# Kernel optimization log

Measured on AMD Instinct MI355X. Metric: run time of the kernel, lower is better.

The kernel has to match this reference:

```python
import jax, jax.numpy as jnp
import numpy as np

TAU = 0.5  # init tau
EPS = 1e-8  # F.cosine_similarity eps


def setup_inputs() -> dict:
    key = jax.random.key(0)
    k1, k2 = jax.random.split(key)
    N, D, NUM_CLASSES = 4096, 1024, 128
    layer_embeds = jax.random.normal(k1, (N, D), dtype=jnp.float32)
    y_true = jax.random.randint(k2, (N,), 0, NUM_CLASSES, dtype=jnp.int64)
    return {"layer_embeds": layer_embeds, "y_true": y_true}


def reference(layer_embeds, y_true):
    N = layer_embeds.shape[0]
    # batched cosine similarity, scaled like the original: (cos + 1) * 0.5 * tau
    norms = jnp.maximum(jnp.linalg.norm(layer_embeds, axis=1), EPS)  # [N]
    cos = (layer_embeds @ layer_embeds.T) / (norms[:, None] * norms[None, :])  # [N, N]
    S = (cos + 1.0) * 0.5 * TAU

    same = y_true[:, None] == y_true[None, :]  # [N, N]
    eye = jnp.eye(N, dtype=bool)
    pos_mask = same & ~eye            # same-label pairs, j != i
    neg_mask = ~same                  # different-label pairs (diag excluded since same there)

    # column 0: first positive (in j order), else stays 0
    has_pos = pos_mask.any(axis=1)
    first_pos = jnp.argmax(pos_mask, axis=1)
    pos_val = jnp.where(has_pos, S[jnp.arange(N), first_pos], 0.0)  # [N]

    # negatives fill columns 1.. in j order: col = 1 + (#negatives with j' < j)
    negi = neg_mask.astype(jnp.int32)
    col = 1 + jnp.cumsum(negi, axis=1) - negi  # [N, N]
    W = 2 * N  # pad one dummy column for non-negative entries
    cols = jnp.where(neg_mask, col, W - 1)
    rows = jnp.broadcast_to(jnp.arange(N)[:, None], (N, N))
    loss_temp = jnp.zeros((N, W), dtype=jnp.float32)
    loss_temp = loss_temp.at[rows, cols].set(jnp.where(neg_mask, S, 0.0))
    loss_temp = loss_temp.at[:, 0].set(pos_val)
    loss_temp = loss_temp[:, : 2 * N - 1]  # [N, 2N-1], matches torch buffer

    # -log_softmax, take column 0, sum over rows, divide by N
    lse = jax.nn.logsumexp(loss_temp, axis=1)  # [N]
    loss = jnp.sum(lse - loss_temp[:, 0]) / N
    return loss
```

## Files before the change

kernel.cpp:

```cpp
#include <hip/hip_runtime.h>
#include <hip/hip_bf16.h>
#include <math.h>

#define NN 4096
#define DD 1024
#define NCLS 128
#define TAU 0.5f
#define EPSV 1e-8f
#define NB_GEMM 528

typedef __bf16 bf16;
typedef __bf16 bf16x8 __attribute__((ext_vector_type(8)));
typedef __bf16 bf16x4 __attribute__((ext_vector_type(4)));
typedef float f32x4 __attribute__((ext_vector_type(4)));

__device__ __forceinline__ void gl2lds16(const void* g, void* l) {
    __builtin_amdgcn_global_load_lds(
        (const __attribute__((address_space(1))) void*)g,
        (__attribute__((address_space(3))) void*)l,
        16, 0, 0);
}

__global__ __launch_bounds__(256) void k_prep(const float* __restrict__ X,
                                              const int* __restrict__ y,
                                              bf16* __restrict__ Xn,
                                              float* __restrict__ rsum,
                                              float* __restrict__ posv,
                                              int* __restrict__ cnt,
                                              int* __restrict__ fpos) {
    const int t = threadIdx.x;
    if (blockIdx.x == 0) {
        __shared__ int sc[NCLS], s1[NCLS], s2[NCLS];
        if (t < NCLS) { sc[t] = 0; s1[t] = 0x7fffffff; s2[t] = 0x7fffffff; }
        __syncthreads();
        int yv[16];
#pragma unroll
        for (int k = 0; k < 16; ++k) {
            int i = t + k * 256;
            yv[k] = y[i];
            atomicAdd(&sc[yv[k]], 1);
            atomicMin(&s1[yv[k]], i);
        }
        __syncthreads();
#pragma unroll
        for (int k = 0; k < 16; ++k) {
            int i = t + k * 256;
            if (s1[yv[k]] != i) atomicMin(&s2[yv[k]], i);
        }
        __syncthreads();
#pragma unroll
        for (int k = 0; k < 16; ++k) {
            int i = t + k * 256;
            int c = yv[k];
            fpos[i] = (sc[c] >= 2) ? (s1[c] == i ? s2[c] : s1[c]) : -1;
        }
        if (t < NCLS) cnt[t] = sc[t];
        return;
    }
    const int w = t >> 6, lane = t & 63;
    const int row = (blockIdx.x - 1) * 4 + w;
    const float* xr = X + (size_t)row * DD;
    float4 v[4];
    float ss = 0.f;
#pragma unroll
    for (int c = 0; c < 4; ++c) {
        v[c] = *(const float4*)(xr + c * 256 + lane * 4);
        ss += v[c].x * v[c].x + v[c].y * v[c].y + v[c].z * v[c].z + v[c].w * v[c].w;
    }
#pragma unroll
    for (int m = 1; m < 64; m <<= 1) ss += __shfl_xor(ss, m, 64);
    float rn = 1.f / fmaxf(sqrtf(ss), EPSV);
    if (lane == 0) { rsum[row] = 0.f; posv[row] = 0.f; }
#pragma unroll
    for (int c = 0; c < 4; ++c) {
        bf16x4 o;
        o.x = (bf16)(v[c].x * rn);
        o.y = (bf16)(v[c].y * rn);
        o.z = (bf16)(v[c].z * rn);
        o.w = (bf16)(v[c].w * rn);
        *(bf16x4*)(Xn + (size_t)row * DD + c * 256 + lane * 4) = o;
    }
}

__global__ __launch_bounds__(256) void k_gemm(const bf16* __restrict__ Xn,
                                              const int* __restrict__ y,
                                              const int* __restrict__ fpos,
                                              float* __restrict__ rowsum,
                                              float* __restrict__ posv) {
    __shared__ __align__(16) bf16 As[128 * 32];
    __shared__ __align__(16) bf16 Bs[128 * 32];
    __shared__ int yA[128], yB[128], fA[128], fB[128];

    int id = (blockIdx.x & 7) * 66 + (blockIdx.x >> 3);
    float ff = sqrtf((float)(8 * id + 1));
    int bj = (int)((ff - 1.f) * 0.5f);
    if (bj * (bj + 1) / 2 > id) bj--;
    if ((bj + 1) * (bj + 2) / 2 <= id) bj++;
    int bi = id - bj * (bj + 1) / 2;
    const int rowA0 = bi * 128;
    const int rowB0 = bj * 128;
    const bool diag = (bi == bj);

    const int tid = threadIdx.x;
    if (tid < 128) { yA[tid] = y[rowA0 + tid]; fA[tid] = fpos[rowA0 + tid]; }
    else { yB[tid - 128] = y[rowB0 + tid - 128]; fB[tid - 128] = fpos[rowB0 + tid - 128]; }

    const int lane = tid & 63;
    const int w = tid >> 6;
    const int wm = w & 1, wn = w >> 1;
    const int lr = lane >> 4, lc = lane & 15;

    f32x4 acc[4][4];
#pragma unroll
    for (int i = 0; i < 4; ++i)
#pragma unroll
        for (int j = 0; j < 4; ++j) acc[i][j] = (f32x4){0.f, 0.f, 0.f, 0.f};

    const int r = tid >> 2;
    const int g = tid & 3;
    const int kg = g ^ ((r >> 1) & 3);
    const bf16* gA0 = Xn + (size_t)(rowA0 + r) * DD + kg * 8;
    const bf16* gA1 = gA0 + (size_t)64 * DD;
    const bf16* gB0 = Xn + (size_t)(rowB0 + r) * DD + kg * 8;
    const bf16* gB1 = gB0 + (size_t)64 * DD;
    bf16* lA0 = As + tid * 8;
    bf16* lA1 = As + 64 * 32 + tid * 8;
    bf16* lB0 = Bs + tid * 8;
    bf16* lB1 = Bs + 64 * 32 + tid * 8;

    const int sw = (lc >> 1) & 3;

    for (int k0 = 0; k0 < DD; k0 += 32) {
        __syncthreads();
        gl2lds16(gA0 + k0, lA0);
        gl2lds16(gA1 + k0, lA1);
        gl2lds16(gB0 + k0, lB0);
        gl2lds16(gB1 + k0, lB1);
        __syncthreads();

        bf16x8 af[4], bfr[4];
#pragma unroll
        for (int mt = 0; mt < 4; ++mt)
            af[mt] = *(const bf16x8*)(As + (wm * 64 + mt * 16 + lc) * 32 + ((lr ^ sw) * 8));
#pragma unroll
        for (int nt = 0; nt < 4; ++nt)
            bfr[nt] = *(const bf16x8*)(Bs + (wn * 64 + nt * 16 + lc) * 32 + ((lr ^ sw) * 8));
#pragma unroll
        for (int mt = 0; mt < 4; ++mt)
#pragma unroll
            for (int nt = 0; nt < 4; ++nt)
                acc[mt][nt] = __builtin_amdgcn_mfma_f32_16x16x32_bf16(
                    af[mt], bfr[nt], acc[mt][nt], 0, 0, 0);
    }

    int cloc[4], ycol[4], fcol[4];
    bool pcol[4];
#pragma unroll
    for (int nt = 0; nt < 4; ++nt) {
        cloc[nt] = wn * 64 + nt * 16 + lc;
        ycol[nt] = yB[cloc[nt]];
        fcol[nt] = fB[cloc[nt]];
        pcol[nt] = ((unsigned)(fcol[nt] - rowA0) < 128u);
    }
    float colacc[4] = {0.f, 0.f, 0.f, 0.f};
#pragma unroll
    for (int mt = 0; mt < 4; ++mt) {
#pragma unroll
        for (int rr = 0; rr < 4; ++rr) {
            int rloc = wm * 64 + mt * 16 + lr * 4 + rr;
            int rglob = rowA0 + rloc;
            int yrow = yA[rloc];
            int fprow = fA[rloc];
            bool prow = ((unsigned)(fprow - rowB0) < 128u);
            float s = 0.f;
#pragma unroll
            for (int nt = 0; nt < 4; ++nt) {
                float Sv = (acc[mt][nt][rr] + 1.f) * (0.5f * TAU);
                int cg = rowB0 + cloc[nt];
                if (prow && cg == fprow) posv[rglob] = Sv;
                if (pcol[nt] && fcol[nt] == rglob) posv[cg] = Sv;
                float e = (ycol[nt] != yrow) ? __expf(Sv) : 0.f;
                s += e;
                colacc[nt] += e;
            }
            s += __shfl_xor(s, 1, 16);
            s += __shfl_xor(s, 2, 16);
            s += __shfl_xor(s, 4, 16);
            s += __shfl_xor(s, 8, 16);
            if (lc == 0) atomicAdd(&rowsum[rglob], s);
        }
    }
    if (!diag) {
#pragma unroll
        for (int nt = 0; nt < 4; ++nt) {
            float cs = colacc[nt];
            cs += __shfl_xor(cs, 16, 64);
            cs += __shfl_xor(cs, 32, 64);
            if (lane < 16) atomicAdd(&rowsum[rowB0 + wn * 64 + nt * 16 + lane], cs);
        }
    }
}

__global__ __launch_bounds__(1024) void k_finalize(const float* __restrict__ rowsum,
                                                   const float* __restrict__ posv,
                                                   const int* __restrict__ y,
                                                   const int* __restrict__ cnt,
                                                   float* __restrict__ out) {
    int t = threadIdx.x;
    float acc = 0.f;
#pragma unroll
    for (int k = 0; k < 4; ++k) {
        int i = t + k * 1024;
        float pv = posv[i];
        float tot = rowsum[i] + __expf(pv) + (float)(NN - 2 + cnt[y[i]]);
        acc += logf(tot) - pv;
    }
#pragma unroll
    for (int m = 1; m < 64; m <<= 1) acc += __shfl_xor(acc, m, 64);
    __shared__ float wsum[16];
    int w = t >> 6, lane = t & 63;
    if (lane == 0) wsum[w] = acc;
    __syncthreads();
    if (t == 0) {
        float s = 0.f;
#pragma unroll
        for (int q = 0; q < 16; ++q) s += wsum[q];
        *out = s / (float)NN;
    }
}

extern "C" void kernel_launch(void* const* d_in, const int* in_sizes, int n_in,
                              void* d_out, int out_size, void* d_ws, size_t ws_size,
                              hipStream_t stream) {
    const float* X = (const float*)d_in[0];
    const int* y = (const int*)d_in[1];
    float* out = (float*)d_out;

    char* ws = (char*)d_ws;
    bf16* Xn    = (bf16*)ws;
    float* rsum = (float*)(ws + 8 * 1024 * 1024);
    float* posv = (float*)(ws + 8 * 1024 * 1024 + 16 * 1024);
    int* cnt    = (int*)(ws + 8 * 1024 * 1024 + 32 * 1024);
    int* fpos   = (int*)(ws + 8 * 1024 * 1024 + 36 * 1024);

    k_prep<<<dim3(NN / 4 + 1), 256, 0, stream>>>(X, y, Xn, rsum, posv, cnt, fpos);
    k_gemm<<<dim3(NB_GEMM), 256, 0, stream>>>(Xn, y, fpos, rsum, posv);
    k_finalize<<<dim3(1), 1024, 0, stream>>>(rsum, posv, y, cnt, out);
}
```

Baseline: 104.0 us.

## Double-buffer LDS tiles and split GEMM block across eight waves

The GEMM kernel now uses 512 threads (8 waves) per 128x128 tile. Each wave computes a 64x32 sub-tile instead of 64x64, which halves the accumulator registers per thread. The LDS tiles are double-buffered so the next K-slice is prefetched with global_load_lds while MFMAs run on the current one, leaving one barrier per iteration instead of two. This aims to hide global-load latency and raise occupancy, at the cost of twice the LDS use and more LDS fragment reads per MFMA.

```diff
diff --git a/kernel.cpp b/kernel.cpp
--- a/kernel.cpp
+++ b/kernel.cpp
@@ -82,13 +82,13 @@
     }
 }
 
-__global__ __launch_bounds__(256) void k_gemm(const bf16* __restrict__ Xn,
-                                              const int* __restrict__ y,
-                                              const int* __restrict__ fpos,
-                                              float* __restrict__ rowsum,
-                                              float* __restrict__ posv) {
-    __shared__ __align__(16) bf16 As[128 * 32];
-    __shared__ __align__(16) bf16 Bs[128 * 32];
+__global__ __launch_bounds__(512, 4) void k_gemm(const bf16* __restrict__ Xn,
+                                                 const int* __restrict__ y,
+                                                 const int* __restrict__ fpos,
+                                                 float* __restrict__ rowsum,
+                                                 float* __restrict__ posv) {
+    __shared__ __align__(16) bf16 As[2][128 * 32];
+    __shared__ __align__(16) bf16 Bs[2][128 * 32];
     __shared__ int yA[128], yB[128], fA[128], fB[128];
 
     int id = (blockIdx.x & 7) * 66 + (blockIdx.x >> 3);
@@ -103,66 +103,65 @@
 
     const int tid = threadIdx.x;
     if (tid < 128) { yA[tid] = y[rowA0 + tid]; fA[tid] = fpos[rowA0 + tid]; }
-    else { yB[tid - 128] = y[rowB0 + tid - 128]; fB[tid - 128] = fpos[rowB0 + tid - 128]; }
+    else if (tid < 256) { yB[tid - 128] = y[rowB0 + tid - 128]; fB[tid - 128] = fpos[rowB0 + tid - 128]; }
 
     const int lane = tid & 63;
     const int w = tid >> 6;
     const int wm = w & 1, wn = w >> 1;
     const int lr = lane >> 4, lc = lane & 15;
 
-    f32x4 acc[4][4];
+    f32x4 acc[4][2];
 #pragma unroll
     for (int i = 0; i < 4; ++i)
 #pragma unroll
-        for (int j = 0; j < 4; ++j) acc[i][j] = (f32x4){0.f, 0.f, 0.f, 0.f};
+        for (int j = 0; j < 2; ++j) acc[i][j] = (f32x4){0.f, 0.f, 0.f, 0.f};
 
     const int r = tid >> 2;
     const int g = tid & 3;
     const int kg = g ^ ((r >> 1) & 3);
-    const bf16* gA0 = Xn + (size_t)(rowA0 + r) * DD + kg * 8;
-    const bf16* gA1 = gA0 + (size_t)64 * DD;
-    const bf16* gB0 = Xn + (size_t)(rowB0 + r) * DD + kg * 8;
-    const bf16* gB1 = gB0 + (size_t)64 * DD;
-    bf16* lA0 = As + tid * 8;
-    bf16* lA1 = As + 64 * 32 + tid * 8;
-    bf16* lB0 = Bs + tid * 8;
-    bf16* lB1 = Bs + 64 * 32 + tid * 8;
+    const bf16* gA = Xn + (size_t)(rowA0 + r) * DD + kg * 8;
+    const bf16* gB = Xn + (size_t)(rowB0 + r) * DD + kg * 8;
+    const int loff = tid * 8;
 
     const int sw = (lc >> 1) & 3;
 
+    gl2lds16(gA, &As[0][loff]);
+    gl2lds16(gB, &Bs[0][loff]);
+    __syncthreads();
+
+    int cur = 0;
     for (int k0 = 0; k0 < DD; k0 += 32) {
-        __syncthreads();
-        gl2lds16(gA0 + k0, lA0);
-        gl2lds16(gA1 + k0, lA1);
-        gl2lds16(gB0 + k0, lB0);
-        gl2lds16(gB1 + k0, lB1);
-        __syncthreads();
-
-        bf16x8 af[4], bfr[4];
+        if (k0 + 32 < DD) {
+            gl2lds16(gA + k0 + 32, &As[cur ^ 1][loff]);
+            gl2lds16(gB + k0 + 32, &Bs[cur ^ 1][loff]);
+        }
+        bf16x8 af[4], bfr[2];
 #pragma unroll
         for (int mt = 0; mt < 4; ++mt)
-            af[mt] = *(const bf16x8*)(As + (wm * 64 + mt * 16 + lc) * 32 + ((lr ^ sw) * 8));
-#pragma unroll
-        for (int nt = 0; nt < 4; ++nt)
-            bfr[nt] = *(const bf16x8*)(Bs + (wn * 64 + nt * 16 + lc) * 32 + ((lr ^ sw) * 8));
+            af[mt] = *(const bf16x8*)(&As[cur][(wm * 64 + mt * 16 + lc) * 32 + ((lr ^ sw) * 8)]);
+#pragma unroll
+        for (int nt = 0; nt < 2; ++nt)
+            bfr[nt] = *(const bf16x8*)(&Bs[cur][(wn * 32 + nt * 16 + lc) * 32 + ((lr ^ sw) * 8)]);
 #pragma unroll
         for (int mt = 0; mt < 4; ++mt)
 #pragma unroll
-            for (int nt = 0; nt < 4; ++nt)
+            for (int nt = 0; nt < 2; ++nt)
                 acc[mt][nt] = __builtin_amdgcn_mfma_f32_16x16x32_bf16(
                     af[mt], bfr[nt], acc[mt][nt], 0, 0, 0);
-    }
-
-    int cloc[4], ycol[4], fcol[4];
-    bool pcol[4];
-#pragma unroll
-    for (int nt = 0; nt < 4; ++nt) {
-        cloc[nt] = wn * 64 + nt * 16 + lc;
+        __syncthreads();
+        cur ^= 1;
+    }
+
+    int cloc[2], ycol[2], fcol[2];
+    bool pcol[2];
+#pragma unroll
+    for (int nt = 0; nt < 2; ++nt) {
+        cloc[nt] = wn * 32 + nt * 16 + lc;
         ycol[nt] = yB[cloc[nt]];
         fcol[nt] = fB[cloc[nt]];
         pcol[nt] = ((unsigned)(fcol[nt] - rowA0) < 128u);
     }
-    float colacc[4] = {0.f, 0.f, 0.f, 0.f};
+    float colacc[2] = {0.f, 0.f};
 #pragma unroll
     for (int mt = 0; mt < 4; ++mt) {
 #pragma unroll
@@ -174,7 +173,7 @@
             bool prow = ((unsigned)(fprow - rowB0) < 128u);
             float s = 0.f;
 #pragma unroll
-            for (int nt = 0; nt < 4; ++nt) {
+            for (int nt = 0; nt < 2; ++nt) {
                 float Sv = (acc[mt][nt][rr] + 1.f) * (0.5f * TAU);
                 int cg = rowB0 + cloc[nt];
                 if (prow && cg == fprow) posv[rglob] = Sv;
@@ -192,11 +191,11 @@
     }
     if (!diag) {
 #pragma unroll
-        for (int nt = 0; nt < 4; ++nt) {
+        for (int nt = 0; nt < 2; ++nt) {
             float cs = colacc[nt];
             cs += __shfl_xor(cs, 16, 64);
             cs += __shfl_xor(cs, 32, 64);
-            if (lane < 16) atomicAdd(&rowsum[rowB0 + wn * 64 + nt * 16 + lane], cs);
+            if (lane < 16) atomicAdd(&rowsum[rowB0 + wn * 32 + nt * 16 + lane], cs);
         }
     }
 }
@@ -244,6 +243,6 @@
     int* fpos   = (int*)(ws + 8 * 1024 * 1024 + 36 * 1024);
 
     k_prep<<<dim3(NN / 4 + 1), 256, 0, stream>>>(X, y, Xn, rsum, posv, cnt, fpos);
-    k_gemm<<<dim3(NB_GEMM), 256, 0, stream>>>(Xn, y, fpos, rsum, posv);
+    k_gemm<<<dim3(NB_GEMM), 512, 0, stream>>>(Xn, y, fpos, rsum, posv);
     k_finalize<<<dim3(1), 1024, 0, stream>>>(rsum, posv, y, cnt, out);
 }
```

Result: slower. 112.7 us (+8.4%).

## Compute full Gram matrix with 256x256 double-buffered tiles instead of triangular

Applied to the files above, without the earlier changes.

Replaces the symmetric triangular 128x128 tiling (528 blocks, with column-sum atomics) by a full 16x16 grid of 256x256 tiles with 512 threads. Global-to-LDS loads are double-buffered with explicit waitcnt/barriers so copies overlap the MFMA work, and MFMA issue priority is raised. This drops the symmetry trick, so twice the matmul FLOPs are done in exchange for larger tiles, fewer atomics, simpler epilogue and latency hiding. The epilogue now reads labels and first-positive indices straight from global memory instead of LDS.

```diff
diff --git a/kernel.cpp b/kernel.cpp
--- a/kernel.cpp
+++ b/kernel.cpp
@@ -7,7 +7,8 @@
 #define NCLS 128
 #define TAU 0.5f
 #define EPSV 1e-8f
-#define NB_GEMM 528
+#define NB_GEMM 256
+#define NT 32
 
 typedef __bf16 bf16;
 typedef __bf16 bf16x8 __attribute__((ext_vector_type(8)));
@@ -82,37 +83,28 @@
     }
 }
 
-__global__ __launch_bounds__(256) void k_gemm(const bf16* __restrict__ Xn,
-                                              const int* __restrict__ y,
-                                              const int* __restrict__ fpos,
-                                              float* __restrict__ rowsum,
-                                              float* __restrict__ posv) {
-    __shared__ __align__(16) bf16 As[128 * 32];
-    __shared__ __align__(16) bf16 Bs[128 * 32];
-    __shared__ int yA[128], yB[128], fA[128], fB[128];
-
-    int id = (blockIdx.x & 7) * 66 + (blockIdx.x >> 3);
-    float ff = sqrtf((float)(8 * id + 1));
-    int bj = (int)((ff - 1.f) * 0.5f);
-    if (bj * (bj + 1) / 2 > id) bj--;
-    if ((bj + 1) * (bj + 2) / 2 <= id) bj++;
-    int bi = id - bj * (bj + 1) / 2;
-    const int rowA0 = bi * 128;
-    const int rowB0 = bj * 128;
-    const bool diag = (bi == bj);
+__global__ __launch_bounds__(512, 2) void k_gemm(const bf16* __restrict__ Xn,
+                                                 const int* __restrict__ y,
+                                                 const int* __restrict__ fpos,
+                                                 float* __restrict__ rowsum,
+                                                 float* __restrict__ posv) {
+    __shared__ __align__(16) bf16 As[2][256 * 32];
+    __shared__ __align__(16) bf16 Bs[2][256 * 32];
+
+    const int id = (blockIdx.x & 7) * 32 + (blockIdx.x >> 3);
+    const int rowA0 = (id >> 4) * 256;
+    const int rowB0 = (id & 15) * 256;
 
     const int tid = threadIdx.x;
-    if (tid < 128) { yA[tid] = y[rowA0 + tid]; fA[tid] = fpos[rowA0 + tid]; }
-    else { yB[tid - 128] = y[rowB0 + tid - 128]; fB[tid - 128] = fpos[rowB0 + tid - 128]; }
-
     const int lane = tid & 63;
     const int w = tid >> 6;
     const int wm = w & 1, wn = w >> 1;
     const int lr = lane >> 4, lc = lane & 15;
-
-    f32x4 acc[4][4];
-#pragma unroll
-    for (int i = 0; i < 4; ++i)
+    const int sw = (lc >> 1) & 3;
+
+    f32x4 acc[8][4];
+#pragma unroll
+    for (int i = 0; i < 8; ++i)
 #pragma unroll
         for (int j = 0; j < 4; ++j) acc[i][j] = (f32x4){0.f, 0.f, 0.f, 0.f};
 
@@ -120,83 +112,78 @@
     const int g = tid & 3;
     const int kg = g ^ ((r >> 1) & 3);
     const bf16* gA0 = Xn + (size_t)(rowA0 + r) * DD + kg * 8;
-    const bf16* gA1 = gA0 + (size_t)64 * DD;
+    const bf16* gA1 = gA0 + (size_t)128 * DD;
     const bf16* gB0 = Xn + (size_t)(rowB0 + r) * DD + kg * 8;
-    const bf16* gB1 = gB0 + (size_t)64 * DD;
-    bf16* lA0 = As + tid * 8;
-    bf16* lA1 = As + 64 * 32 + tid * 8;
-    bf16* lB0 = Bs + tid * 8;
-    bf16* lB1 = Bs + 64 * 32 + tid * 8;
-
-    const int sw = (lc >> 1) & 3;
-
-    for (int k0 = 0; k0 < DD; k0 += 32) {
-        __syncthreads();
-        gl2lds16(gA0 + k0, lA0);
-        gl2lds16(gA1 + k0, lA1);
-        gl2lds16(gB0 + k0, lB0);
-        gl2lds16(gB1 + k0, lB1);
-        __syncthreads();
-
-        bf16x8 af[4], bfr[4];
-#pragma unroll
-        for (int mt = 0; mt < 4; ++mt)
-            af[mt] = *(const bf16x8*)(As + (wm * 64 + mt * 16 + lc) * 32 + ((lr ^ sw) * 8));
+    const bf16* gB1 = gB0 + (size_t)128 * DD;
+    const int loff = tid * 8;
+
+    auto stage = [&](int buf, int k0) {
+        gl2lds16(gA0 + k0, &As[buf][loff]);
+        gl2lds16(gA1 + k0, &As[buf][4096 + loff]);
+        gl2lds16(gB0 + k0, &Bs[buf][loff]);
+        gl2lds16(gB1 + k0, &Bs[buf][4096 + loff]);
+    };
+    auto compute = [&](int buf) {
+        bf16x8 af[8], bfr[4];
+#pragma unroll
+        for (int mt = 0; mt < 8; ++mt)
+            af[mt] = *(const bf16x8*)(&As[buf][(wm * 128 + mt * 16 + lc) * 32 + ((lr ^ sw) * 8)]);
 #pragma unroll
         for (int nt = 0; nt < 4; ++nt)
-            bfr[nt] = *(const bf16x8*)(Bs + (wn * 64 + nt * 16 + lc) * 32 + ((lr ^ sw) * 8));
-#pragma unroll
-        for (int mt = 0; mt < 4; ++mt)
+            bfr[nt] = *(const bf16x8*)(&Bs[buf][(wn * 64 + nt * 16 + lc) * 32 + ((lr ^ sw) * 8)]);
+        __builtin_amdgcn_s_setprio(1);
+#pragma unroll
+        for (int mt = 0; mt < 8; ++mt)
 #pragma unroll
             for (int nt = 0; nt < 4; ++nt)
                 acc[mt][nt] = __builtin_amdgcn_mfma_f32_16x16x32_bf16(
                     af[mt], bfr[nt], acc[mt][nt], 0, 0, 0);
-    }
-
-    int cloc[4], ycol[4], fcol[4];
-    bool pcol[4];
+        __builtin_amdgcn_s_setprio(0);
+    };
+
+    stage(0, 0);
+
+#pragma unroll 2
+    for (int t = 0; t < NT - 1; ++t) {
+        const int cur = t & 1;
+        stage(cur ^ 1, (t + 1) * 32);
+        asm volatile("s_waitcnt vmcnt(4)" ::: "memory");
+        __builtin_amdgcn_s_barrier();
+        compute(cur);
+        asm volatile("s_waitcnt lgkmcnt(0)" ::: "memory");
+        __builtin_amdgcn_s_barrier();
+    }
+    asm volatile("s_waitcnt vmcnt(0)" ::: "memory");
+    __builtin_amdgcn_s_barrier();
+    compute((NT - 1) & 1);
+
+    int ycol[4], cloc[4];
 #pragma unroll
     for (int nt = 0; nt < 4; ++nt) {
         cloc[nt] = wn * 64 + nt * 16 + lc;
-        ycol[nt] = yB[cloc[nt]];
-        fcol[nt] = fB[cloc[nt]];
-        pcol[nt] = ((unsigned)(fcol[nt] - rowA0) < 128u);
-    }
-    float colacc[4] = {0.f, 0.f, 0.f, 0.f};
-#pragma unroll
-    for (int mt = 0; mt < 4; ++mt) {
+        ycol[nt] = y[rowB0 + cloc[nt]];
+    }
+#pragma unroll
+    for (int mt = 0; mt < 8; ++mt) {
 #pragma unroll
         for (int rr = 0; rr < 4; ++rr) {
-            int rloc = wm * 64 + mt * 16 + lr * 4 + rr;
+            int rloc = wm * 128 + mt * 16 + lr * 4 + rr;
             int rglob = rowA0 + rloc;
-            int yrow = yA[rloc];
-            int fprow = fA[rloc];
-            bool prow = ((unsigned)(fprow - rowB0) < 128u);
+            int yrow = y[rglob];
+            int fprow = fpos[rglob];
+            bool prow = ((unsigned)(fprow - rowB0) < 256u);
             float s = 0.f;
 #pragma unroll
             for (int nt = 0; nt < 4; ++nt) {
                 float Sv = (acc[mt][nt][rr] + 1.f) * (0.5f * TAU);
-                int cg = rowB0 + cloc[nt];
-                if (prow && cg == fprow) posv[rglob] = Sv;
-                if (pcol[nt] && fcol[nt] == rglob) posv[cg] = Sv;
-                float e = (ycol[nt] != yrow) ? __expf(Sv) : 0.f;
-                s += e;
-                colacc[nt] += e;
+                if (prow && rowB0 + cloc[nt] == fprow) posv[rglob] = Sv;
+                s += (ycol[nt] != yrow) ? __expf(Sv) : 0.f;
             }
             s += __shfl_xor(s, 1, 16);
             s += __shfl_xor(s, 2, 16);
             s += __shfl_xor(s, 4, 16);
             s += __shfl_xor(s, 8, 16);
             if (lc == 0) atomicAdd(&rowsum[rglob], s);
-        }
-    }
-    if (!diag) {
-#pragma unroll
-        for (int nt = 0; nt < 4; ++nt) {
-            float cs = colacc[nt];
-            cs += __shfl_xor(cs, 16, 64);
-            cs += __shfl_xor(cs, 32, 64);
-            if (lane < 16) atomicAdd(&rowsum[rowB0 + wn * 64 + nt * 16 + lane], cs);
         }
     }
 }
@@ -244,6 +231,6 @@
     int* fpos   = (int*)(ws + 8 * 1024 * 1024 + 36 * 1024);
 
     k_prep<<<dim3(NN / 4 + 1), 256, 0, stream>>>(X, y, Xn, rsum, posv, cnt, fpos);
-    k_gemm<<<dim3(NB_GEMM), 256, 0, stream>>>(Xn, y, fpos, rsum, posv);
+    k_gemm<<<dim3(NB_GEMM), 512, 0, stream>>>(Xn, y, fpos, rsum, posv);
     k_finalize<<<dim3(1), 1024, 0, stream>>>(rsum, posv, y, cnt, out);
 }
```

Result: slower. 126.3 us (+21.5%).
